# Optimization experiments

Measured on AMD Instinct MI355X. Metric: run time of the kernel, lower is better.

Reference implementation:

```python
import jax, jax.numpy as jnp
import numpy as np

D_MODEL = 1024
H = 16
D_K = D_MODEL // H


def setup_inputs() -> dict:
    key = jax.random.key(0)
    ks = jax.random.split(key, 8)
    B, S = 2, 2048
    scale = 1.0 / np.sqrt(D_MODEL)
    return {
        "query": jax.random.normal(ks[0], (B, S, D_MODEL), dtype=jnp.float32),
        "key": jax.random.normal(ks[1], (B, S, D_MODEL), dtype=jnp.float32),
        "value": jax.random.normal(ks[2], (B, S, D_MODEL), dtype=jnp.float32),
        "mask": jnp.ones((B, 1, 1, S), dtype=jnp.int32),
        "Wq": jax.random.normal(ks[3], (D_MODEL, D_MODEL), dtype=jnp.float32) * scale,
        "Wk": jax.random.normal(ks[4], (D_MODEL, D_MODEL), dtype=jnp.float32) * scale,
        "Wv": jax.random.normal(ks[5], (D_MODEL, D_MODEL), dtype=jnp.float32) * scale,
        "Wo": jax.random.normal(ks[6], (D_MODEL, D_MODEL), dtype=jnp.float32) * scale,
    }


def reference(query, key, value, mask, Wq, Wk, Wv, Wo):
    # mask is a no-op in the original (masked_fill result discarded); dropout=0.
    B, S, _ = query.shape
    q = (query @ Wq.T).reshape(B, S, H, D_K)  # [B,S,H,Dk]
    k = (key @ Wk.T).reshape(B, S, H, D_K)
    v = (value @ Wv.T).reshape(B, S, H, D_K)
    # scores = Q K^T / sqrt(d_k)  -- NOTE: no softmax in the source module
    scores = jnp.einsum("bqhd,bkhd->bhqk", q, k) / jnp.sqrt(jnp.float32(D_K))
    out = jnp.einsum("bhqk,bkhd->bqhd", scores, v).reshape(B, S, D_MODEL)
    return out @ Wo.T
```

## Files before the change

kernel.cpp:

```cpp
#include <hip/hip_runtime.h>

#define DEV __device__ __forceinline__

typedef __attribute__((ext_vector_type(8))) short short8;
typedef __attribute__((ext_vector_type(4))) float f32x4;

DEV short f2bf(float x) {
  unsigned u = __float_as_uint(x);
  unsigned r = (u + 0x7fffu + ((u >> 16) & 1u)) >> 16;
  return (short)r;
}
DEV float bf2f(short x) {
  return __uint_as_float(((unsigned)(unsigned short)x) << 16);
}

DEV void gload_lds16(const void* g, void* l) {
  __builtin_amdgcn_global_load_lds((const __attribute__((address_space(1))) void*)g,
                                   (__attribute__((address_space(3))) void*)l, 16, 0, 0);
}

__global__ __launch_bounds__(256) void cvt_all(
    const float* __restrict__ s0, const float* __restrict__ s1,
    const float* __restrict__ s2, const float* __restrict__ s3,
    const float* __restrict__ s4, const float* __restrict__ s5,
    const float* __restrict__ s6,
    short* __restrict__ d0, short* __restrict__ d1, short* __restrict__ d2,
    short* __restrict__ d3, short* __restrict__ d4, short* __restrict__ d5,
    short* __restrict__ d6) {
  int g = blockIdx.x * 256 + threadIdx.x;
  const float* s;
  short* d;
  int off;
  if (g < 524288) { s = s0; d = d0; off = g; }
  else if (g < 1048576) { s = s1; d = d1; off = g - 524288; }
  else if (g < 1572864) { s = s2; d = d2; off = g - 1048576; }
  else {
    int w2 = g - 1572864;
    int seg = w2 >> 17;
    off = w2 & 131071;
    s = seg == 0 ? s3 : seg == 1 ? s4 : seg == 2 ? s5 : s6;
    d = seg == 0 ? d3 : seg == 1 ? d4 : seg == 2 ? d5 : d6;
  }
  const float4* p = reinterpret_cast<const float4*>(s) + (size_t)off * 2;
  float4 a = p[0], b = p[1];
  short8 o;
  o[0] = f2bf(a.x); o[1] = f2bf(a.y); o[2] = f2bf(a.z); o[3] = f2bf(a.w);
  o[4] = f2bf(b.x); o[5] = f2bf(b.y); o[6] = f2bf(b.z); o[7] = f2bf(b.w);
  *reinterpret_cast<short8*>(d + (size_t)off * 8) = o;
}

template <typename OutT>
__global__ __launch_bounds__(256) void gemm_bt128(const short* __restrict__ A,
                                                  const short* __restrict__ W,
                                                  OutT* __restrict__ C,
                                                  long strideA, long strideW, long strideC) {
  __shared__ short At[128 * 64];
  __shared__ short Bt[128 * 64];
  const short* Ab = A + (size_t)blockIdx.z * strideA;
  const short* Wb = W + (size_t)blockIdx.z * strideW;
  OutT* Cb = C + (size_t)blockIdx.z * strideC;
  const int t = threadIdx.x;
  const int w = t >> 6;
  const int l = t & 63;
  const int lg = l >> 4, lr = l & 15;
  const int wm = w >> 1, wn = w & 1;
  const int rowBase = blockIdx.y * 128;
  const int colBase = blockIdx.x * 128;

  f32x4 acc[4][4] = {};

  for (int kt = 0; kt < 16; ++kt) {
    const int k0 = kt * 64;
    __syncthreads();
#pragma unroll
    for (int i = 0; i < 4; ++i) {
      int c = w * 256 + i * 64 + l;
      int r = c >> 3, s = c & 7;
      int goff = k0 + ((s ^ (r & 7)) << 3);
      gload_lds16(Ab + (size_t)(rowBase + r) * 1024 + goff, At + (size_t)c * 8);
      gload_lds16(Wb + (size_t)(colBase + r) * 1024 + goff, Bt + (size_t)c * 8);
    }
    __syncthreads();
#pragma unroll
    for (int kk = 0; kk < 2; ++kk) {
      short8 afr[4], bfr[4];
#pragma unroll
      for (int m = 0; m < 4; ++m) {
        int ar = wm * 64 + m * 16 + lr;
        int slot = (kk * 4 + lg) ^ (ar & 7);
        afr[m] = *reinterpret_cast<const short8*>(&At[ar * 64 + slot * 8]);
      }
#pragma unroll
      for (int n = 0; n < 4; ++n) {
        int br = wn * 64 + n * 16 + lr;
        int slot = (kk * 4 + lg) ^ (br & 7);
        bfr[n] = *reinterpret_cast<const short8*>(&Bt[br * 64 + slot * 8]);
      }
#pragma unroll
      for (int m = 0; m < 4; ++m)
#pragma unroll
        for (int n = 0; n < 4; ++n)
          acc[m][n] = __builtin_amdgcn_mfma_f32_16x16x32_bf16(afr[m], bfr[n], acc[m][n], 0, 0, 0);
    }
  }
#pragma unroll
  for (int m = 0; m < 4; ++m)
#pragma unroll
    for (int n = 0; n < 4; ++n) {
      int row0 = rowBase + wm * 64 + m * 16 + lg * 4;
      int col = colBase + wn * 64 + n * 16 + lr;
#pragma unroll
      for (int j = 0; j < 4; ++j) {
        float v = acc[m][n][j];
        if constexpr (sizeof(OutT) == 2)
          Cb[(size_t)(row0 + j) * 1024 + col] = (OutT)f2bf(v);
        else
          Cb[(size_t)(row0 + j) * 1024 + col] = (OutT)v;
      }
    }
}

__global__ __launch_bounds__(256) void kv_outer(const short* __restrict__ Kp,
                                                const short* __restrict__ Vp,
                                                float* __restrict__ Mb) {
  __shared__ float Ks[128][64];
  __shared__ float Vs[128][64];
  const int t = threadIdx.x;
  const int sc = blockIdx.x, h = blockIdx.y, b = blockIdx.z;
  const size_t base = ((size_t)(b * 2048 + sc * 128)) * 1024 + h * 64;
  for (int e = t; e < 128 * 64; e += 256) {
    int r = e >> 6, c = e & 63;
    size_t g = base + (size_t)r * 1024 + c;
    Ks[r][c] = bf2f(Kp[g]);
    Vs[r][c] = bf2f(Vp[g]);
  }
  __syncthreads();
  const int dp0 = (t >> 4) * 4, d0 = (t & 15) * 4;
  float acc[4][4] = {};
  for (int s = 0; s < 128; ++s) {
    float4 kv = *reinterpret_cast<const float4*>(&Ks[s][dp0]);
    float4 vv = *reinterpret_cast<const float4*>(&Vs[s][d0]);
    float ka[4] = {kv.x, kv.y, kv.z, kv.w};
    float va[4] = {vv.x, vv.y, vv.z, vv.w};
#pragma unroll
    for (int i = 0; i < 4; ++i)
#pragma unroll
      for (int j = 0; j < 4; ++j) acc[i][j] += ka[i] * va[j];
  }
  float* dst = Mb + (size_t)(b * 16 + h) * 4096;
#pragma unroll
  for (int i = 0; i < 4; ++i)
#pragma unroll
    for (int j = 0; j < 4; ++j)
      atomicAdd(&dst[(dp0 + i) * 64 + d0 + j], acc[i][j] * 0.125f);
}

__global__ __launch_bounds__(256) void make_w2t(const float* __restrict__ Mb,
                                                const short* __restrict__ Wo,
                                                short* __restrict__ W2T) {
  __shared__ float Ms[64][65];
  __shared__ float Wos[64][64];
  const int t = threadIdx.x;
  const int jc = blockIdx.x, h = blockIdx.y, b = blockIdx.z;
  const float* Msrc = Mb + (size_t)(b * 16 + h) * 4096;
  for (int e = t; e < 4096; e += 256) {
    int r = e >> 6, c = e & 63;
    Ms[r][c] = Msrc[e];
    Wos[r][c] = bf2f(Wo[(size_t)(jc * 64 + r) * 1024 + h * 64 + c]);
  }
  __syncthreads();
  const int j0 = (t >> 4) * 4, p0 = (t & 15) * 4;
  float acc[4][4] = {};
  for (int d = 0; d < 64; ++d) {
    float wv[4], mv[4];
#pragma unroll
    for (int i = 0; i < 4; ++i) { wv[i] = Wos[j0 + i][d]; mv[i] = Ms[p0 + i][d]; }
#pragma unroll
    for (int i = 0; i < 4; ++i)
#pragma unroll
      for (int j2 = 0; j2 < 4; ++j2) acc[i][j2] += wv[i] * mv[j2];
  }
  short* dst = W2T + (size_t)b * 1048576;
#pragma unroll
  for (int i = 0; i < 4; ++i)
#pragma unroll
    for (int j2 = 0; j2 < 4; ++j2)
      dst[(size_t)(jc * 64 + j0 + i) * 1024 + h * 64 + p0 + j2] = f2bf(acc[i][j2]);
}

extern "C" void kernel_launch(void* const* d_in, const int* in_sizes, int n_in,
                              void* d_out, int out_size, void* d_ws, size_t ws_size,
                              hipStream_t stream) {
  const float* q  = (const float*)d_in[0];
  const float* k  = (const float*)d_in[1];
  const float* v  = (const float*)d_in[2];
  const float* Wq = (const float*)d_in[4];
  const float* Wk = (const float*)d_in[5];
  const float* Wv = (const float*)d_in[6];
  const float* Wo = (const float*)d_in[7];
  float* out = (float*)d_out;
  char* ws = (char*)d_ws;

  short* qkv = (short*)(ws);
  short* qb = qkv;
  short* kb = qkv + (size_t)4194304;
  short* vb = qkv + (size_t)8388608;
  short* wb = (short*)(ws + (24l << 20));
  short* wqb = wb;
  short* wkb = wb + 1048576;
  short* wvb = wb + 2097152;
  short* wob = wb + 3145728;
  short* Pp = (short*)(ws + (32l << 20));
  short* Qp = Pp;
  short* Kp = Pp + (size_t)4194304;
  short* Vp = Pp + (size_t)8388608;
  float* Mb  = (float*)(ws + (56l << 20));
  short* W2T = (short*)(ws + (57l << 20));

  hipMemsetAsync(Mb, 0, 32 * 64 * 64 * sizeof(float), stream);

  cvt_all<<<8192, 256, 0, stream>>>(q, k, v, Wq, Wk, Wv, Wo,
                                    qb, kb, vb, wqb, wkb, wvb, wob);

  gemm_bt128<short><<<dim3(8, 32, 3), 256, 0, stream>>>(
      qkv, wb, Pp, 4194304l, 1048576l, 4194304l);

  kv_outer<<<dim3(16, 16, 2), 256, 0, stream>>>(Kp, Vp, Mb);
  make_w2t<<<dim3(16, 16, 2), 256, 0, stream>>>(Mb, wob, W2T);

  gemm_bt128<float><<<dim3(8, 16, 2), 256, 0, stream>>>(
      Qp, W2T, out, 2097152l, 1048576l, 2097152l);
}
```

Baseline: 217.7 us.

## Shrink GEMM N-tile to 64, swizzle block order, fold Mb zeroing into cvt

The GEMM tile becomes 128x64 so each GEMM launches twice as many workgroups (1536 and 512). This is meant to fill the 256 CUs on mi355x, which were underused at 768 and 256 blocks. A flat block index remap spreads adjacent blocks across XCDs for L2 locality. The separate hipMemsetAsync for the Mb accumulator is replaced by extra threads in the conversion kernel, saving one launch. The cost is lower arithmetic intensity per block, since A tiles are now loaded twice as often.

```diff
diff --git a/kernel.cpp b/kernel.cpp
--- a/kernel.cpp
+++ b/kernel.cpp
@@ -26,8 +26,16 @@
     const float* __restrict__ s6,
     short* __restrict__ d0, short* __restrict__ d1, short* __restrict__ d2,
     short* __restrict__ d3, short* __restrict__ d4, short* __restrict__ d5,
-    short* __restrict__ d6) {
+    short* __restrict__ d6, float* __restrict__ Mb) {
   int g = blockIdx.x * 256 + threadIdx.x;
+  if (g >= 2097152) {
+    int off = g - 2097152;
+    float4 z = {0.f, 0.f, 0.f, 0.f};
+    float4* p = reinterpret_cast<float4*>(Mb) + (size_t)off * 2;
+    p[0] = z;
+    p[1] = z;
+    return;
+  }
   const float* s;
   short* d;
   int off;
@@ -50,24 +58,33 @@
 }
 
 template <typename OutT>
-__global__ __launch_bounds__(256) void gemm_bt128(const short* __restrict__ A,
-                                                  const short* __restrict__ W,
-                                                  OutT* __restrict__ C,
-                                                  long strideA, long strideW, long strideC) {
+__global__ __launch_bounds__(256) void gemm_bt64(const short* __restrict__ A,
+                                                 const short* __restrict__ W,
+                                                 OutT* __restrict__ C,
+                                                 long strideA, long strideW, long strideC) {
   __shared__ short At[128 * 64];
-  __shared__ short Bt[128 * 64];
-  const short* Ab = A + (size_t)blockIdx.z * strideA;
-  const short* Wb = W + (size_t)blockIdx.z * strideW;
-  OutT* Cb = C + (size_t)blockIdx.z * strideC;
+  __shared__ short Bt[64 * 64];
+  const int nx = gridDim.x, ny = gridDim.y;
+  int flat = blockIdx.x + nx * (blockIdx.y + ny * blockIdx.z);
+  int nwg = nx * ny * gridDim.z;
+  int l2 = (flat & 7) * (nwg >> 3) + (flat >> 3);
+  int colB = l2 % nx;
+  int tmp = l2 / nx;
+  int rowB = tmp % ny;
+  int zB = tmp / ny;
+
+  const short* Ab = A + (size_t)zB * strideA;
+  const short* Wb = W + (size_t)zB * strideW;
+  OutT* Cb = C + (size_t)zB * strideC;
   const int t = threadIdx.x;
   const int w = t >> 6;
   const int l = t & 63;
   const int lg = l >> 4, lr = l & 15;
   const int wm = w >> 1, wn = w & 1;
-  const int rowBase = blockIdx.y * 128;
-  const int colBase = blockIdx.x * 128;
-
-  f32x4 acc[4][4] = {};
+  const int rowBase = rowB * 128;
+  const int colBase = colB * 64;
+
+  f32x4 acc[4][2] = {};
 
   for (int kt = 0; kt < 16; ++kt) {
     const int k0 = kt * 64;
@@ -76,39 +93,42 @@
     for (int i = 0; i < 4; ++i) {
       int c = w * 256 + i * 64 + l;
       int r = c >> 3, s = c & 7;
-      int goff = k0 + ((s ^ (r & 7)) << 3);
-      gload_lds16(Ab + (size_t)(rowBase + r) * 1024 + goff, At + (size_t)c * 8);
-      gload_lds16(Wb + (size_t)(colBase + r) * 1024 + goff, Bt + (size_t)c * 8);
+      gload_lds16(Ab + (size_t)(rowBase + r) * 1024 + k0 + ((s ^ (r & 7)) << 3),
+                  At + (size_t)c * 8);
+    }
+#pragma unroll
+    for (int i = 0; i < 2; ++i) {
+      int c = w * 128 + i * 64 + l;
+      int r = c >> 3, s = c & 7;
+      gload_lds16(Wb + (size_t)(colBase + r) * 1024 + k0 + ((s ^ (r & 7)) << 3),
+                  Bt + (size_t)c * 8);
     }
     __syncthreads();
 #pragma unroll
     for (int kk = 0; kk < 2; ++kk) {
-      short8 afr[4], bfr[4];
+      short8 bfr[2];
+#pragma unroll
+      for (int n = 0; n < 2; ++n) {
+        int br = wn * 32 + n * 16 + lr;
+        int slot = (kk * 4 + lg) ^ (br & 7);
+        bfr[n] = *reinterpret_cast<const short8*>(&Bt[br * 64 + slot * 8]);
+      }
 #pragma unroll
       for (int m = 0; m < 4; ++m) {
         int ar = wm * 64 + m * 16 + lr;
         int slot = (kk * 4 + lg) ^ (ar & 7);
-        afr[m] = *reinterpret_cast<const short8*>(&At[ar * 64 + slot * 8]);
+        short8 afr = *reinterpret_cast<const short8*>(&At[ar * 64 + slot * 8]);
+        acc[m][0] = __builtin_amdgcn_mfma_f32_16x16x32_bf16(afr, bfr[0], acc[m][0], 0, 0, 0);
+        acc[m][1] = __builtin_amdgcn_mfma_f32_16x16x32_bf16(afr, bfr[1], acc[m][1], 0, 0, 0);
       }
-#pragma unroll
-      for (int n = 0; n < 4; ++n) {
-        int br = wn * 64 + n * 16 + lr;
-        int slot = (kk * 4 + lg) ^ (br & 7);
-        bfr[n] = *reinterpret_cast<const short8*>(&Bt[br * 64 + slot * 8]);
-      }
-#pragma unroll
-      for (int m = 0; m < 4; ++m)
-#pragma unroll
-        for (int n = 0; n < 4; ++n)
-          acc[m][n] = __builtin_amdgcn_mfma_f32_16x16x32_bf16(afr[m], bfr[n], acc[m][n], 0, 0, 0);
     }
   }
 #pragma unroll
   for (int m = 0; m < 4; ++m)
 #pragma unroll
-    for (int n = 0; n < 4; ++n) {
+    for (int n = 0; n < 2; ++n) {
       int row0 = rowBase + wm * 64 + m * 16 + lg * 4;
-      int col = colBase + wn * 64 + n * 16 + lr;
+      int col = colBase + wn * 32 + n * 16 + lr;
 #pragma unroll
       for (int j = 0; j < 4; ++j) {
         float v = acc[m][n][j];
@@ -217,17 +237,16 @@
   float* Mb  = (float*)(ws + (56l << 20));
   short* W2T = (short*)(ws + (57l << 20));
 
-  hipMemsetAsync(Mb, 0, 32 * 64 * 64 * sizeof(float), stream);
-
-  cvt_all<<<8192, 256, 0, stream>>>(q, k, v, Wq, Wk, Wv, Wo,
-                                    qb, kb, vb, wqb, wkb, wvb, wob);
-
-  gemm_bt128<short><<<dim3(8, 32, 3), 256, 0, stream>>>(
+  cvt_all<<<8256, 256, 0, stream>>>(q, k, v, Wq, Wk, Wv, Wo,
+                                    qb, kb, vb, wqb, wkb, wvb, wob, Mb);
+
+  gemm_bt64<short><<<dim3(16, 32, 3), 256, 0, stream>>>(
       qkv, wb, Pp, 4194304l, 1048576l, 4194304l);
 
   kv_outer<<<dim3(16, 16, 2), 256, 0, stream>>>(Kp, Vp, Mb);
+
   make_w2t<<<dim3(16, 16, 2), 256, 0, stream>>>(Mb, wob, W2T);
 
-  gemm_bt128<float><<<dim3(8, 16, 2), 256, 0, stream>>>(
+  gemm_bt64<float><<<dim3(16, 16, 2), 256, 0, stream>>>(
       Qp, W2T, out, 2097152l, 1048576l, 2097152l);
 }
```

Measured after the change: 209.1 us. 4.0% less time.
